# Optimization experiments

Hardware: AMD Instinct MI355X
Metric: run time of the kernel (lower is better)

The kernel has to match this reference:

```python
import jax, jax.numpy as jnp
import numpy as np

TEMPERATURE = 0.5
NEG_INF = -1e9  # used to mask self-similarity diagonal before logsumexp


def setup_inputs() -> dict:
    key = jax.random.key(0)
    k1, k2 = jax.random.split(key)
    N, Z = 4096, 128
    z1 = jax.random.normal(k1, (N, Z), dtype=jnp.float32)
    z2 = jax.random.normal(k2, (N, Z), dtype=jnp.float32)
    return {"z1": z1, "z2": z2}


def reference(z1, z2):
    # NT-Xent (SimCLR) loss. Faithful to:
    #   sim = cosine_similarity over all pairs of concat([z1, z2])
    #   positives = sim diagonals at offsets +-N; negatives = all off-(self)diag entries
    #   cross_entropy with the positive as class 0  ->  -pos/T + logsumexp(all non-self sims / T)
    N = z1.shape[0]
    reps = jnp.concatenate([z1, z2], axis=0)                      # [2N, Z]
    # row-normalize once; cosine sim matrix is then a single GEMM
    norms = jnp.linalg.norm(reps, axis=-1, keepdims=True)
    # torch cosine_similarity clamps norms by eps=1e-8
    nreps = reps / jnp.maximum(norms, 1e-8)
    sim = nreps @ nreps.T                                          # [2N, 2N]
    # positives: sim[i, i+N] for i<N and sim[i, i-N] for i>=N
    l_pos = jnp.diagonal(sim, offset=N)                            # [N]
    r_pos = jnp.diagonal(sim, offset=-N)                           # [N]
    positives = jnp.concatenate([l_pos, r_pos])                    # [2N]
    # logsumexp over all entries except the self-similarity diagonal.
    # (The positive entry stays in the denominator exactly once, matching
    #  concat([positive, negatives]) in the original.)
    two_n = 2 * N
    self_mask = jnp.eye(two_n, dtype=bool)
    logits = jnp.where(self_mask, NEG_INF, sim / TEMPERATURE)      # [2N, 2N]
    lse = jax.nn.logsumexp(logits, axis=1)                         # [2N]
    per_row = lse - positives / TEMPERATURE                        # CE with label 0
    return jnp.sum(per_row) / two_n
```

## Files before the change

### kernel.cpp

```cpp
#include <hip/hip_runtime.h>
#include <hip/hip_bf16.h>


#define N_PAIRS 4096
#define ZDIM    128
#define NROWS   8192
#define QS 1.6986437717f

typedef __bf16 bf16x8 __attribute__((ext_vector_type(8)));
typedef float  floatx4 __attribute__((ext_vector_type(4)));

__global__ __launch_bounds__(256) void k_normalize(
    const float* __restrict__ z1, const float* __restrict__ z2,
    __hip_bfloat16* __restrict__ pack, float* __restrict__ pos,
    float* __restrict__ denom)
{
    const int zi = blockIdx.x * 256 + threadIdx.x;
    if (zi < NROWS) denom[zi] = 0.0f;

    const int w = threadIdx.x >> 6;
    const int lane = threadIdx.x & 63;
    const int p = blockIdx.x * 4 + w;
    const float2 a = ((const float2*)(z1 + (size_t)p * ZDIM))[lane];
    const float2 b = ((const float2*)(z2 + (size_t)p * ZDIM))[lane];
    float s1 = a.x * a.x + a.y * a.y;
    float s2 = b.x * b.x + b.y * b.y;
    float d  = a.x * b.x + a.y * b.y;
    #pragma unroll
    for (int off = 1; off < 64; off <<= 1) {
        s1 += __shfl_xor(s1, off, 64);
        s2 += __shfl_xor(s2, off, 64);
        d  += __shfl_xor(d,  off, 64);
    }
    const float n1 = fmaxf(sqrtf(s1), 1e-8f);
    const float n2 = fmaxf(sqrtf(s2), 1e-8f);
    const float i1 = 1.0f / n1, i2 = 1.0f / n2;
    const float q1 = i1 * QS, q2 = i2 * QS;
    float2 na; na.x = a.x * q1; na.y = a.y * q1;
    float2 nb; nb.x = b.x * q2; nb.y = b.y * q2;

    const int ks = lane >> 4;
    const int qq = (lane >> 2) & 3;
    const int jj = (lane & 3) * 2;
    const int r1 = p, r2 = p + N_PAIRS;
    const size_t i1e = ((size_t)((r1 >> 4) * 4 + ks)) * 512 + qq * 128 + (r1 & 15) * 8 + jj;
    const size_t i2e = ((size_t)((r2 >> 4) * 4 + ks)) * 512 + qq * 128 + (r2 & 15) * 8 + jj;
    *(__hip_bfloat162*)(pack + i1e) = __float22bfloat162_rn(na);
    *(__hip_bfloat162*)(pack + i2e) = __float22bfloat162_rn(nb);
    if (lane == 0) pos[p] = d * i1 * i2;
}

__global__ __launch_bounds__(256) void k_simsum(
    const __hip_bfloat16* __restrict__ pack, float* __restrict__ denom)
{
    const int tid  = threadIdx.x;
    const int lane = tid & 63;
    const int w    = tid >> 6;
    const int rt   = blockIdx.x >> 4;
    const int cs   = blockIdx.x & 15;
    const int q    = lane >> 4;
    const int l16  = lane & 15;

    const int rowb = rt * 256 + w * 64;
    const __hip_bfloat16* Abase =
        pack + ((size_t)(rowb >> 4) * 4) * 512 + lane * 8;
    bf16x8 afrag[4][4];
    #pragma unroll
    for (int mt = 0; mt < 4; ++mt)
        #pragma unroll
        for (int ks = 0; ks < 4; ++ks)
            afrag[mt][ks] = *(const bf16x8*)(Abase + mt * 2048 + ks * 512);

    float rowsum[4][4];
    #pragma unroll
    for (int mt = 0; mt < 4; ++mt)
        #pragma unroll
        for (int r = 0; r < 4; ++r) rowsum[mt][r] = 0.0f;

    const __hip_bfloat16* Bcol0 =
        pack + ((size_t)((cs * 512) >> 4) * 4) * 512 + lane * 8;

    auto loadB = [&](bf16x8 (&buf)[4][2], int hs) {
        const __hip_bfloat16* bp = Bcol0 + (size_t)hs * 4096;
        #pragma unroll
        for (int ks = 0; ks < 4; ++ks)
            #pragma unroll
            for (int nt = 0; nt < 2; ++nt)
                buf[ks][nt] = *(const bf16x8*)(bp + nt * 2048 + ks * 512);
    };

    auto compute = [&](bf16x8 (&buf)[4][2], int hs) {
        floatx4 acc[4][2];
        #pragma unroll
        for (int mt = 0; mt < 4; ++mt)
            #pragma unroll
            for (int nt = 0; nt < 2; ++nt) {
                acc[mt][nt].x = 0.f; acc[mt][nt].y = 0.f;
                acc[mt][nt].z = 0.f; acc[mt][nt].w = 0.f;
            }
        #pragma unroll
        for (int ks = 0; ks < 4; ++ks)
            #pragma unroll
            for (int mt = 0; mt < 4; ++mt)
                #pragma unroll
                for (int nt = 0; nt < 2; ++nt)
                    acc[mt][nt] = __builtin_amdgcn_mfma_f32_16x16x32_bf16(
                        afrag[mt][ks], buf[ks][nt], acc[mt][nt], 0, 0, 0);
        const int colb = cs * 512 + hs * 32;
        #pragma unroll
        for (int mt = 0; mt < 4; ++mt) {
            const int rowtb = rowb + mt * 16;
            #pragma unroll
            for (int nt = 0; nt < 2; ++nt) {
                const int coltb = colb + nt * 16;
                if (rowtb == coltb) {
                    #pragma unroll
                    for (int r = 0; r < 4; ++r) {
                        const float e = __builtin_amdgcn_exp2f(acc[mt][nt][r]);
                        rowsum[mt][r] += (l16 == q * 4 + r) ? 0.0f : e;
                    }
                } else {
                    #pragma unroll
                    for (int r = 0; r < 4; ++r)
                        rowsum[mt][r] += __builtin_amdgcn_exp2f(acc[mt][nt][r]);
                }
            }
        }
    };

    bf16x8 bufA[4][2], bufB[4][2];
    loadB(bufA, 0);
    for (int hs = 0; hs < 16; hs += 2) {
        loadB(bufB, hs + 1);
        compute(bufA, hs);
        loadB(bufA, (hs + 2) & 15);
        compute(bufB, hs + 1);
    }

    #pragma unroll
    for (int mt = 0; mt < 4; ++mt)
        #pragma unroll
        for (int r = 0; r < 4; ++r) {
            float s = rowsum[mt][r];
            s += __shfl_xor(s, 1, 64);
            s += __shfl_xor(s, 2, 64);
            s += __shfl_xor(s, 4, 64);
            s += __shfl_xor(s, 8, 64);
            rowsum[mt][r] = s;
        }
    if (l16 == 0) {
        #pragma unroll
        for (int mt = 0; mt < 4; ++mt)
            #pragma unroll
            for (int r = 0; r < 4; ++r) {
                const int grow = rowb + mt * 16 + q * 4 + r;
                atomicAdd(&denom[grow], rowsum[mt][r]);
            }
    }
}

__global__ __launch_bounds__(1024) void k_finish(
    const float* __restrict__ denom, const float* __restrict__ pos,
    float* __restrict__ out)
{
    __shared__ float red[16];
    const int t = threadIdx.x;
    const int lane = t & 63, wv = t >> 6;
    float s = 0.0f;
    for (int i = t; i < NROWS; i += 1024) s += __logf(denom[i]);
    float p = 0.0f;
    for (int i = t; i < N_PAIRS; i += 1024) p += pos[i];
    float v = s - 4.0f * p;
    #pragma unroll
    for (int off = 1; off < 64; off <<= 1) v += __shfl_xor(v, off, 64);
    if (lane == 0) red[wv] = v;
    __syncthreads();
    if (wv == 0) {
        float x = (lane < 16) ? red[lane] : 0.0f;
        #pragma unroll
        for (int off = 1; off < 16; off <<= 1) x += __shfl_xor(x, off, 64);
        if (lane == 0) out[0] = x / (float)NROWS;
    }
}

extern "C" void kernel_launch(void* const* d_in, const int* in_sizes, int n_in,
                              void* d_out, int out_size, void* d_ws, size_t ws_size,
                              hipStream_t stream) {
    const float* z1 = (const float*)d_in[0];
    const float* z2 = (const float*)d_in[1];
    float* out = (float*)d_out;

    char* ws = (char*)d_ws;
    __hip_bfloat16* pack = (__hip_bfloat16*)ws;
    float* denom = (float*)(ws + (size_t)NROWS * ZDIM * 2);
    float* pos   = denom + NROWS;

    k_normalize<<<N_PAIRS / 4, 256, 0, stream>>>(z1, z2, pack, pos, denom);
    k_simsum<<<512, 256, 0, stream>>>(pack, denom);
    k_finish<<<1, 1024, 0, stream>>>(denom, pos, out);
}
```

Measured before the change: 85.68 us.

## Exploit similarity matrix symmetry with triangular work split across blocks

```diff
diff --git a/kernel.cpp b/kernel.cpp
--- a/kernel.cpp
+++ b/kernel.cpp
@@ -56,32 +56,20 @@
     const int tid  = threadIdx.x;
     const int lane = tid & 63;
     const int w    = tid >> 6;
-    const int rt   = blockIdx.x >> 4;
-    const int cs   = blockIdx.x & 15;
     const int q    = lane >> 4;
     const int l16  = lane & 15;
 
-    const int rowb = rt * 256 + w * 64;
-    const __hip_bfloat16* Abase =
-        pack + ((size_t)(rowb >> 4) * 4) * 512 + lane * 8;
-    bf16x8 afrag[4][4];
-    #pragma unroll
-    for (int mt = 0; mt < 4; ++mt)
-        #pragma unroll
-        for (int ks = 0; ks < 4; ++ks)
-            afrag[mt][ks] = *(const bf16x8*)(Abase + mt * 2048 + ks * 512);
-
-    float rowsum[4][4];
-    #pragma unroll
-    for (int mt = 0; mt < 4; ++mt)
-        #pragma unroll
-        for (int r = 0; r < 4; ++r) rowsum[mt][r] = 0.0f;
-
-    const __hip_bfloat16* Bcol0 =
-        pack + ((size_t)((cs * 512) >> 4) * 4) * 512 + lane * 8;
-
-    auto loadB = [&](bf16x8 (&buf)[4][2], int hs) {
-        const __hip_bfloat16* bp = Bcol0 + (size_t)hs * 4096;
+    const int b  = blockIdx.x;
+    int u        = (33 * b) >> 2;
+    const int u1 = (33 * b + 33) >> 2;
+
+    int rt = 0, snext = 256;
+    while (u >= snext) { ++rt; snext += 256 - 8 * rt; }
+
+    bf16x8 bufA[4][2], bufB[4][2];
+
+    auto loadB = [&](bf16x8 (&buf)[4][2], int col) {
+        const __hip_bfloat16* bp = pack + (size_t)col * 128 + lane * 8;
         #pragma unroll
         for (int ks = 0; ks < 4; ++ks)
             #pragma unroll
@@ -89,73 +77,114 @@
                 buf[ks][nt] = *(const bf16x8*)(bp + nt * 2048 + ks * 512);
     };
 
-    auto compute = [&](bf16x8 (&buf)[4][2], int hs) {
-        floatx4 acc[4][2];
+    while (u < u1) {
+        const int srt  = snext - (256 - 8 * rt);
+        const int uend = (u1 < snext) ? u1 : snext;
+        const int rowb = rt * 256 + w * 64;
+
+        const __hip_bfloat16* Abase = pack + (size_t)rowb * 128 + lane * 8;
+        bf16x8 afrag[4][4];
         #pragma unroll
         for (int mt = 0; mt < 4; ++mt)
             #pragma unroll
-            for (int nt = 0; nt < 2; ++nt) {
-                acc[mt][nt].x = 0.f; acc[mt][nt].y = 0.f;
-                acc[mt][nt].z = 0.f; acc[mt][nt].w = 0.f;
-            }
-        #pragma unroll
-        for (int ks = 0; ks < 4; ++ks)
+            for (int ks = 0; ks < 4; ++ks)
+                afrag[mt][ks] = *(const bf16x8*)(Abase + mt * 2048 + ks * 512);
+
+        float rowsum[4][4];
+        #pragma unroll
+        for (int mt = 0; mt < 4; ++mt)
+            #pragma unroll
+            for (int r = 0; r < 4; ++r) rowsum[mt][r] = 0.0f;
+
+        auto compute = [&](bf16x8 (&buf)[4][2], int ur) {
+            const int  col  = rt * 256 + ur * 32;
+            const bool band = (ur < 8);
+            floatx4 acc[4][2];
             #pragma unroll
             for (int mt = 0; mt < 4; ++mt)
                 #pragma unroll
-                for (int nt = 0; nt < 2; ++nt)
-                    acc[mt][nt] = __builtin_amdgcn_mfma_f32_16x16x32_bf16(
-                        afrag[mt][ks], buf[ks][nt], acc[mt][nt], 0, 0, 0);
-        const int colb = cs * 512 + hs * 32;
-        #pragma unroll
-        for (int mt = 0; mt < 4; ++mt) {
-            const int rowtb = rowb + mt * 16;
-            #pragma unroll
-            for (int nt = 0; nt < 2; ++nt) {
-                const int coltb = colb + nt * 16;
-                if (rowtb == coltb) {
+                for (int nt = 0; nt < 2; ++nt) {
+                    acc[mt][nt].x = 0.f; acc[mt][nt].y = 0.f;
+                    acc[mt][nt].z = 0.f; acc[mt][nt].w = 0.f;
+                }
+            #pragma unroll
+            for (int ks = 0; ks < 4; ++ks)
+                #pragma unroll
+                for (int mt = 0; mt < 4; ++mt)
                     #pragma unroll
-                    for (int r = 0; r < 4; ++r) {
-                        const float e = __builtin_amdgcn_exp2f(acc[mt][nt][r]);
-                        rowsum[mt][r] += (l16 == q * 4 + r) ? 0.0f : e;
+                    for (int nt = 0; nt < 2; ++nt)
+                        acc[mt][nt] = __builtin_amdgcn_mfma_f32_16x16x32_bf16(
+                            afrag[mt][ks], buf[ks][nt], acc[mt][nt], 0, 0, 0);
+            float cp0 = 0.0f, cp1 = 0.0f;
+            #pragma unroll
+            for (int mt = 0; mt < 4; ++mt) {
+                const int rowtb = rowb + mt * 16;
+                #pragma unroll
+                for (int nt = 0; nt < 2; ++nt) {
+                    const int coltb = col + nt * 16;
+                    if (band && rowtb == coltb) {
+                        #pragma unroll
+                        for (int r = 0; r < 4; ++r) {
+                            const float e = __builtin_amdgcn_exp2f(acc[mt][nt][r]);
+                            rowsum[mt][r] += (l16 == q * 4 + r) ? 0.0f : e;
+                        }
+                    } else {
+                        #pragma unroll
+                        for (int r = 0; r < 4; ++r) {
+                            const float e = __builtin_amdgcn_exp2f(acc[mt][nt][r]);
+                            rowsum[mt][r] += e;
+                            if (!band) { if (nt == 0) cp0 += e; else cp1 += e; }
+                        }
                     }
-                } else {
-                    #pragma unroll
-                    for (int r = 0; r < 4; ++r)
-                        rowsum[mt][r] += __builtin_amdgcn_exp2f(acc[mt][nt][r]);
                 }
             }
+            if (!band) {
+                cp0 += __shfl_xor(cp0, 16, 64);
+                cp0 += __shfl_xor(cp0, 32, 64);
+                cp1 += __shfl_xor(cp1, 16, 64);
+                cp1 += __shfl_xor(cp1, 32, 64);
+                if (q == 0) {
+                    atomicAdd(&denom[col + l16], cp0);
+                    atomicAdd(&denom[col + 16 + l16], cp1);
+                }
+            }
+        };
+
+        int ur        = u - srt;
+        const int urn = uend - srt;
+        loadB(bufA, rt * 256 + ur * 32);
+        while (ur + 2 <= urn) {
+            loadB(bufB, rt * 256 + (ur + 1) * 32);
+            compute(bufA, ur);
+            int nx = ur + 2;
+            if (nx >= urn) nx = urn - 1;
+            loadB(bufA, rt * 256 + nx * 32);
+            compute(bufB, ur + 1);
+            ur += 2;
         }
-    };
-
-    bf16x8 bufA[4][2], bufB[4][2];
-    loadB(bufA, 0);
-    for (int hs = 0; hs < 16; hs += 2) {
-        loadB(bufB, hs + 1);
-        compute(bufA, hs);
-        loadB(bufA, (hs + 2) & 15);
-        compute(bufB, hs + 1);
-    }
-
-    #pragma unroll
-    for (int mt = 0; mt < 4; ++mt)
-        #pragma unroll
-        for (int r = 0; r < 4; ++r) {
-            float s = rowsum[mt][r];
-            s += __shfl_xor(s, 1, 64);
-            s += __shfl_xor(s, 2, 64);
-            s += __shfl_xor(s, 4, 64);
-            s += __shfl_xor(s, 8, 64);
-            rowsum[mt][r] = s;
+        if (ur < urn) compute(bufA, ur);
+
+        #pragma unroll
+        for (int mt = 0; mt < 4; ++mt)
+            #pragma unroll
+            for (int r = 0; r < 4; ++r) {
+                float s = rowsum[mt][r];
+                s += __shfl_xor(s, 1, 64);
+                s += __shfl_xor(s, 2, 64);
+                s += __shfl_xor(s, 4, 64);
+                s += __shfl_xor(s, 8, 64);
+                rowsum[mt][r] = s;
+            }
+        if (l16 == 0) {
+            #pragma unroll
+            for (int mt = 0; mt < 4; ++mt)
+                #pragma unroll
+                for (int r = 0; r < 4; ++r)
+                    atomicAdd(&denom[rowb + mt * 16 + q * 4 + r], rowsum[mt][r]);
         }
-    if (l16 == 0) {
-        #pragma unroll
-        for (int mt = 0; mt < 4; ++mt)
-            #pragma unroll
-            for (int r = 0; r < 4; ++r) {
-                const int grow = rowb + mt * 16 + q * 4 + r;
-                atomicAdd(&denom[grow], rowsum[mt][r]);
-            }
+
+        u = uend;
+        if (u < u1) { ++rt; snext += 256 - 8 * rt; }
     }
 }
 
```

Measured after the change: 82.14 us. 1.04x faster.
